# Kernel optimization log

Hardware: AMD Instinct MI355X
Metric: run time of the kernel (lower is better)

## Reference

```python
import jax, jax.numpy as jnp
import numpy as np

N, E, D = 100000, 1600000, 128


def setup_inputs() -> dict:
    key = jax.random.key(0)
    ks = jax.random.split(key, 8)
    s = 1.0 / np.sqrt(D)
    return {
        "x": jax.random.normal(ks[0], (N, D), dtype=jnp.float32),
        "edge_index": jax.random.randint(ks[1], (2, E), 0, N, dtype=jnp.int64),
        "x_prev": jax.random.normal(ks[2], (N, D), dtype=jnp.float32),
        # GCNConv params: weight [in,out], bias [out]
        "W": jax.random.uniform(ks[3], (D, D), jnp.float32, -s, s),
        "b": jnp.zeros((D,), jnp.float32),
        # GRUCell params (torch layout): [3*H, H] gates ordered (r, z, n)
        "W_ih": jax.random.uniform(ks[4], (3 * D, D), jnp.float32, -s, s),
        "W_hh": jax.random.uniform(ks[5], (3 * D, D), jnp.float32, -s, s),
        "b_ih": jax.random.uniform(ks[6], (3 * D,), jnp.float32, -s, s),
        "b_hh": jax.random.uniform(ks[7], (3 * D,), jnp.float32, -s, s),
    }


def _gcn_conv(x, edge_index, W, b):
    n = x.shape[0]
    loop = jnp.arange(n, dtype=edge_index.dtype)
    src = jnp.concatenate([edge_index[0], loop])  # [E+N]
    dst = jnp.concatenate([edge_index[1], loop])
    # symmetric normalization: deg over destinations (incl. self loops)
    deg = jax.ops.segment_sum(jnp.ones_like(dst, dtype=x.dtype), dst, num_segments=n)
    dinv = jnp.where(deg > 0, jax.lax.rsqrt(deg), 0.0)
    norm = dinv[src] * dinv[dst]  # [E+N]
    xw = x @ W  # [N, out]
    msg = xw[src] * norm[:, None]  # gather + scale
    return jax.ops.segment_sum(msg, dst, num_segments=n) + b


def _gru_cell(inp, h, W_ih, W_hh, b_ih, b_hh):
    gi = inp @ W_ih.T + b_ih  # [N, 3H]
    gh = h @ W_hh.T + b_hh
    i_r, i_z, i_n = jnp.split(gi, 3, axis=-1)
    h_r, h_z, h_n = jnp.split(gh, 3, axis=-1)
    r = jax.nn.sigmoid(i_r + h_r)
    z = jax.nn.sigmoid(i_z + h_z)
    ntil = jnp.tanh(i_n + r * h_n)
    return (1.0 - z) * ntil + z * h


def reference(x, edge_index, x_prev, W, b, W_ih, W_hh, b_ih, b_hh):
    h_cur = _gcn_conv(x, edge_index, W, b)
    return _gru_cell(h_cur, x_prev, W_ih, W_hh, b_ih, b_hh)
```

## Files before the change

kernel.cpp:

```cpp
#include <hip/hip_runtime.h>
#include <hip/hip_bf16.h>
#include <math.h>

#define DIM 128
#define PSHIFT 10
#define PSZ 1024
#define CHUNK 2048

typedef __attribute__((ext_vector_type(8))) short bf16x8;
typedef __attribute__((ext_vector_type(4))) float f32x4;
typedef unsigned short u16;
typedef unsigned int u32;
typedef unsigned long long u64;

__device__ __forceinline__ u16 f2bf(float x) {
    u32 u = __builtin_bit_cast(u32, x);
    u += 0x7fff + ((u >> 16) & 1);
    return (u16)(u >> 16);
}
__device__ __forceinline__ float bf2f(u16 h) {
    return __builtin_bit_cast(float, (u32)h << 16);
}
__device__ __forceinline__ float fsig(float x) {
    return __builtin_amdgcn_rcpf(1.f + __expf(-x));
}
__device__ __forceinline__ float ftanh(float x) {
    return 1.f - 2.f * __builtin_amdgcn_rcpf(__expf(2.f * x) + 1.f);
}


__global__ __launch_bounds__(256) void k_zero(int* __restrict__ p, int n) {
    int i = blockIdx.x * 256 + threadIdx.x;
    if (i < n) p[i] = 0;
}

__global__ __launch_bounds__(256) void k_pcount(const int* __restrict__ edst,
                                                int* __restrict__ pcnt, int E) {
    __shared__ int h[128];
    int t = threadIdx.x;
    if (t < 128) h[t] = 0;
    __syncthreads();
    int stride = gridDim.x * 256;
    for (int e = blockIdx.x * 256 + t; e < E; e += stride)
        atomicAdd(&h[edst[e] >> PSHIFT], 1);
    __syncthreads();
    if (t < 128 && h[t]) atomicAdd(&pcnt[t], h[t]);
}

__global__ __launch_bounds__(256) void k_pscan(const int* __restrict__ pcnt,
                                               int* __restrict__ poff,
                                               int* __restrict__ pfill,
                                               int* __restrict__ rowp,
                                               int P, int N, int E) {
    __shared__ int a[256];
    int t = threadIdx.x;
    int v = (t < P) ? pcnt[t] : 0;
    a[t] = v;
    __syncthreads();
    #pragma unroll
    for (int off = 1; off < 256; off <<= 1) {
        int y = (t >= off) ? a[t - off] : 0;
        __syncthreads();
        a[t] += y;
        __syncthreads();
    }
    int excl = a[t] - v;
    if (t < P) { poff[t] = excl; pfill[t] = excl; }
    if (t == 0) { poff[P] = E; rowp[N] = E; }
}

__global__ __launch_bounds__(256) void k_pscatter(const int* __restrict__ esrc,
                                                  const int* __restrict__ edst,
                                                  int* __restrict__ pfill,
                                                  u64* __restrict__ pbuf, int E) {
    __shared__ int hist[128], sc[128], lofs[128], gbase[128];
    __shared__ u32 ss[CHUNK], sd[CHUNK];
    int t = threadIdx.x;
    int c0 = blockIdx.x * CHUNK;
    int cnt = E - c0; if (cnt > CHUNK) cnt = CHUNK;

    if (t < 128) hist[t] = 0;
    __syncthreads();

    u32 s[8], d[8];
    int p[8], r[8];
    #pragma unroll
    for (int j = 0; j < 8; ++j) {
        int i = j * 256 + t;
        if (i < cnt) {
            s[j] = (u32)esrc[c0 + i];
            d[j] = (u32)edst[c0 + i];
            p[j] = (int)(d[j] >> PSHIFT);
            r[j] = atomicAdd(&hist[p[j]], 1);
        }
    }
    __syncthreads();

    if (t < 128) sc[t] = hist[t];
    __syncthreads();
    #pragma unroll
    for (int off = 1; off < 128; off <<= 1) {
        int y = 0;
        if (t < 128 && t >= off) y = sc[t - off];
        __syncthreads();
        if (t < 128) sc[t] += y;
        __syncthreads();
    }
    if (t < 128) {
        lofs[t] = sc[t] - hist[t];
        if (hist[t] > 0) gbase[t] = atomicAdd(&pfill[t], hist[t]);
    }
    __syncthreads();

    #pragma unroll
    for (int j = 0; j < 8; ++j) {
        int i = j * 256 + t;
        if (i < cnt) {
            int idx = lofs[p[j]] + r[j];
            ss[idx] = s[j];
            sd[idx] = d[j];
        }
    }
    __syncthreads();

    for (int i = t; i < cnt; i += 256) {
        u32 dd = sd[i];
        int pp = (int)(dd >> PSHIFT);
        int gpos = gbase[pp] + (i - lofs[pp]);
        pbuf[gpos] = (u64)ss[i] | ((u64)dd << 32);
    }
}

__global__ __launch_bounds__(256) void k_pfill(const u64* __restrict__ pbuf,
                                               const int* __restrict__ poff,
                                               int* __restrict__ rowp,
                                               int* __restrict__ srcs,
                                               float* __restrict__ dinv, int N) {
    __shared__ int cnt[PSZ];
    __shared__ int wsum[4];
    int p = blockIdx.x, t = threadIdx.x;
    int lane = t & 63, wid = t >> 6;
    int nb0 = p << PSHIFT;
    int ncnt = N - nb0; if (ncnt > PSZ) ncnt = PSZ;
    int b0 = poff[p], b1 = poff[p + 1];
    int bc = b1 - b0;

    for (int i = t; i < PSZ; i += 256) cnt[i] = 0;
    __syncthreads();
    for (int i = t; i < bc; i += 256) {
        u32 d = (u32)(pbuf[b0 + i] >> 32);
        atomicAdd(&cnt[d - nb0], 1);
    }
    __syncthreads();

    int base = t * 4;
    int c[4];
    int ssum = 0;
    #pragma unroll
    for (int j = 0; j < 4; ++j) { c[j] = cnt[base + j]; ssum += c[j]; }
    int incl = ssum;
    #pragma unroll
    for (int off = 1; off < 64; off <<= 1) {
        int y = __shfl_up(incl, off, 64);
        if (lane >= off) incl += y;
    }
    if (lane == 63) wsum[wid] = incl;
    __syncthreads();
    int add = 0;
    for (int w = 0; w < wid; ++w) add += wsum[w];
    int rr = b0 + add + (incl - ssum);
    #pragma unroll
    for (int j = 0; j < 4; ++j) {
        int i = base + j;
        if (i < ncnt) {
            rowp[nb0 + i] = rr;
            dinv[nb0 + i] = rsqrtf((float)(c[j] + 1));
        }
        cnt[i] = rr;
        rr += c[j];
    }
    __syncthreads();

    for (int i = t; i < bc; i += 256) {
        u64 v = pbuf[b0 + i];
        u32 sv = (u32)v;
        u32 d = (u32)(v >> 32);
        int pos = atomicAdd(&cnt[d - nb0], 1);
        srcs[pos] = (int)sv;
    }
}


__global__ __launch_bounds__(256) void k_prep(const float* __restrict__ W,
                                              const float* __restrict__ Wih,
                                              const float* __restrict__ Whh,
                                              const float4* __restrict__ xp,
                                              u16* __restrict__ Wt,
                                              u16* __restrict__ Wihb,
                                              u16* __restrict__ Whhb,
                                              u32* __restrict__ Xpb, int n4) {
    int gid = blockIdx.x * 256 + threadIdx.x;
    int stride = gridDim.x * 256;
    for (int i = gid; i < n4; i += stride) {
        float4 v = xp[i];
        Xpb[i * 2 + 0] = (u32)f2bf(v.x) | ((u32)f2bf(v.y) << 16);
        Xpb[i * 2 + 1] = (u32)f2bf(v.z) | ((u32)f2bf(v.w) << 16);
    }
    if (gid < 128 * 128) {
        int k = gid >> 7, c = gid & 127;
        Wt[c * 128 + k] = f2bf(W[gid]);
    }
    if (gid < 3 * 128 * 128) {
        Wihb[gid] = f2bf(Wih[gid]);
        Whhb[gid] = f2bf(Whh[gid]);
    }
}


__global__ __launch_bounds__(256) void k_gemm1(const float* __restrict__ X,
                                               const u16* __restrict__ Wt,
                                               u16* __restrict__ XWb, int n) {
    __shared__ u16 Wlds[128 * 128];
    int t = threadIdx.x, w = t >> 6, l = t & 63;
    int lr = l & 15, q = l >> 4;

    for (int cidx = t; cidx < 2048; cidx += 256) {
        int r = cidx >> 4, kc = cidx & 15;
        int dst = r * 128 + ((kc * 8) ^ ((r & 7) << 3));
        *(bf16x8*)(Wlds + dst) = *(const bf16x8*)(Wt + r * 128 + kc * 8);
    }
    __syncthreads();

    int r0 = blockIdx.x * 128;
    int wrow0 = r0 + w * 32;
    int sw = (lr & 7) << 3;
    int ar0 = wrow0 + lr;      if (ar0 > n - 1) ar0 = n - 1;
    int ar1 = wrow0 + 16 + lr; if (ar1 > n - 1) ar1 = n - 1;
    const float* x0 = X + (size_t)ar0 * DIM;
    const float* x1 = X + (size_t)ar1 * DIM;

    f32x4 acc[2][8];
    #pragma unroll
    for (int s = 0; s < 2; ++s)
        #pragma unroll
        for (int c = 0; c < 8; ++c) acc[s][c] = (f32x4){0.f, 0.f, 0.f, 0.f};

    #pragma unroll
    for (int kb = 0; kb < 4; ++kb) {
        int ko = kb * 32 + q * 8;
        float4 f00 = *(const float4*)(x0 + ko), f01 = *(const float4*)(x0 + ko + 4);
        float4 f10 = *(const float4*)(x1 + ko), f11 = *(const float4*)(x1 + ko + 4);
        bf16x8 a0, a1;
        a0[0] = (short)f2bf(f00.x); a0[1] = (short)f2bf(f00.y);
        a0[2] = (short)f2bf(f00.z); a0[3] = (short)f2bf(f00.w);
        a0[4] = (short)f2bf(f01.x); a0[5] = (short)f2bf(f01.y);
        a0[6] = (short)f2bf(f01.z); a0[7] = (short)f2bf(f01.w);
        a1[0] = (short)f2bf(f10.x); a1[1] = (short)f2bf(f10.y);
        a1[2] = (short)f2bf(f10.z); a1[3] = (short)f2bf(f10.w);
        a1[4] = (short)f2bf(f11.x); a1[5] = (short)f2bf(f11.y);
        a1[6] = (short)f2bf(f11.z); a1[7] = (short)f2bf(f11.w);
        int kw = ko ^ sw;
        #pragma unroll
        for (int ct = 0; ct < 8; ++ct) {
            bf16x8 b = *(const bf16x8*)(Wlds + (ct * 16 + lr) * 128 + kw);
            acc[0][ct] = __builtin_amdgcn_mfma_f32_16x16x32_bf16(a0, b, acc[0][ct], 0, 0, 0);
            acc[1][ct] = __builtin_amdgcn_mfma_f32_16x16x32_bf16(a1, b, acc[1][ct], 0, 0, 0);
        }
    }

    #pragma unroll
    for (int s = 0; s < 2; ++s)
        #pragma unroll
        for (int ct = 0; ct < 8; ++ct)
            #pragma unroll
            for (int i = 0; i < 4; ++i) {
                int row = wrow0 + s * 16 + q * 4 + i;
                if (row < n)
                    XWb[(size_t)row * DIM + ct * 16 + lr] = f2bf(acc[s][ct][i]);
            }
}


__global__ __launch_bounds__(256) void k_gather(const u16* __restrict__ XWb,
                                                const float* __restrict__ dinv,
                                                const int* __restrict__ row_ptr,
                                                const int* __restrict__ srcs,
                                                const float* __restrict__ bias,
                                                u16* __restrict__ Hcb, int n) {
    int node = blockIdx.x * 4 + (threadIdx.x >> 6);
    if (node >= n) return;
    int lane = threadIdx.x & 63;
    int c = lane * 2;

    float di = dinv[node];
    u32 sv = *(const u32*)(XWb + (size_t)node * DIM + c);
    float accx = bias[c]     + bf2f((u16)(sv & 0xffff)) * di * di;
    float accy = bias[c + 1] + bf2f((u16)(sv >> 16))    * di * di;

    int e = row_ptr[node], end = row_ptr[node + 1];
    for (; e + 7 < end; e += 8) {
        int sdx[8]; float nw[8]; u32 vv[8];
        #pragma unroll
        for (int j = 0; j < 8; ++j) sdx[j] = srcs[e + j];
        #pragma unroll
        for (int j = 0; j < 8; ++j) nw[j] = dinv[sdx[j]] * di;
        #pragma unroll
        for (int j = 0; j < 8; ++j)
            vv[j] = *(const u32*)(XWb + (size_t)sdx[j] * DIM + c);
        #pragma unroll
        for (int j = 0; j < 8; ++j) {
            accx += bf2f((u16)(vv[j] & 0xffff)) * nw[j];
            accy += bf2f((u16)(vv[j] >> 16)) * nw[j];
        }
    }
    for (; e < end; ++e) {
        int s = srcs[e];
        float nrm = dinv[s] * di;
        u32 v = *(const u32*)(XWb + (size_t)s * DIM + c);
        accx += bf2f((u16)(v & 0xffff)) * nrm;
        accy += bf2f((u16)(v >> 16)) * nrm;
    }
    *(u32*)(Hcb + (size_t)node * DIM + c) = (u32)f2bf(accx) | ((u32)f2bf(accy) << 16);
}


__global__ __launch_bounds__(256) void k_gru(const u16* __restrict__ Hcb,
                                             const u16* __restrict__ Xpb,
                                             const u16* __restrict__ Wihb,
                                             const u16* __restrict__ Whhb,
                                             const float* __restrict__ bih,
                                             const float* __restrict__ bhh,
                                             float* __restrict__ Out, int n) {
    __shared__ u16 Wlds[96 * 128];
    int t = threadIdx.x, w = t >> 6, l = t & 63;
    int lr = l & 15, q = l >> 4;

    int nwg = gridDim.x;
    int qq = nwg >> 3, rr8 = nwg & 7;
    int xcd = blockIdx.x & 7, idx = blockIdx.x >> 3;
    int logical = (xcd < rr8 ? xcd * (qq + 1) : rr8 * (qq + 1) + (xcd - rr8) * qq) + idx;
    int cs = logical & 7;
    int slot = logical >> 3;
    int nslot = nwg >> 3;
    int c0 = cs * 16;

    for (int cidx = t; cidx < 1536; cidx += 256) {
        int r = cidx >> 4, kc = cidx & 15;
        int m = (r >= 48);
        int rr = m ? r - 48 : r;
        int g = rr >> 4, cc = rr & 15;
        const u16* src = (m ? Whhb : Wihb) + (size_t)((g << 7) + c0 + cc) * DIM + kc * 8;
        int dst = r * 128 + ((kc * 8) ^ ((r & 7) << 3));
        *(bf16x8*)(Wlds + dst) = *(const bf16x8*)src;
    }
    __syncthreads();

    int sw = (lr & 7) << 3;
    int j = c0 + lr;
    float br = bih[j],       bz = bih[128 + j], bn = bih[256 + j];
    float cr = bhh[j],       cz = bhh[128 + j], cn = bhh[256 + j];

    int nrb = (n + 63) >> 6;
    for (int rb = slot; rb < nrb; rb += nslot) {
        int wrow0 = rb * 64 + w * 16;
        int ar = wrow0 + lr; if (ar > n - 1) ar = n - 1;
        const u16* hb = Hcb + (size_t)ar * DIM;
        const u16* xb = Xpb + (size_t)ar * DIM;

        u16 hp16[4];
        #pragma unroll
        for (int i = 0; i < 4; ++i) {
            int row = wrow0 + q * 4 + i; if (row > n - 1) row = n - 1;
            hp16[i] = Xpb[(size_t)row * DIM + j];
        }

        f32x4 aI[3], aH[3];
        #pragma unroll
        for (int g = 0; g < 3; ++g) {
            aI[g] = (f32x4){0.f, 0.f, 0.f, 0.f};
            aH[g] = (f32x4){0.f, 0.f, 0.f, 0.f};
        }

        #pragma unroll
        for (int kb = 0; kb < 4; ++kb) {
            int ko = kb * 32 + q * 8;
            bf16x8 hA = *(const bf16x8*)(hb + ko);
            bf16x8 xA = *(const bf16x8*)(xb + ko);
            int kw = ko ^ sw;
            #pragma unroll
            for (int g = 0; g < 3; ++g) {
                int ridx = (g * 16 + lr) * 128 + kw;
                bf16x8 bI = *(const bf16x8*)(Wlds + ridx);
                bf16x8 bH = *(const bf16x8*)(Wlds + ridx + 48 * 128);
                aI[g] = __builtin_amdgcn_mfma_f32_16x16x32_bf16(hA, bI, aI[g], 0, 0, 0);
                aH[g] = __builtin_amdgcn_mfma_f32_16x16x32_bf16(xA, bH, aH[g], 0, 0, 0);
            }
        }

        #pragma unroll
        for (int i = 0; i < 4; ++i) {
            int row = wrow0 + q * 4 + i;
            if (row >= n) continue;
            float ir = aI[0][i] + br;
            float iz = aI[1][i] + bz;
            float in_ = aI[2][i] + bn;
            float hr = aH[0][i] + cr;
            float hz = aH[1][i] + cz;
            float hn = aH[2][i] + cn;
            float rg = fsig(ir + hr);
            float zg = fsig(iz + hz);
            float ng = ftanh(in_ + rg * hn);
            float hp = bf2f(hp16[i]);
            Out[(size_t)row * DIM + j] = (1.f - zg) * ng + zg * hp;
        }
    }
}


extern "C" void kernel_launch(void* const* d_in, const int* in_sizes, int n_in,
                              void* d_out, int out_size, void* d_ws, size_t ws_size,
                              hipStream_t stream) {
    const float* x     = (const float*)d_in[0];
    const int*   ei    = (const int*)d_in[1];
    const float* xprev = (const float*)d_in[2];
    const float* W     = (const float*)d_in[3];
    const float* b     = (const float*)d_in[4];
    const float* Wih   = (const float*)d_in[5];
    const float* Whh   = (const float*)d_in[6];
    const float* bih   = (const float*)d_in[7];
    const float* bhh   = (const float*)d_in[8];

    int N = in_sizes[0] / DIM;
    int E = in_sizes[1] / 2;
    int P = (N + PSZ - 1) >> PSHIFT;
    const int* esrc = ei;
    const int* edst = ei + E;

    char* p = (char*)d_ws;
    auto alloc = [&](size_t bytes) {
        char* q = p;
        p += (bytes + 255) & ~(size_t)255;
        return q;
    };
    float* dinv = (float*)alloc((size_t)N * 4);
    int*   rowp = (int*)  alloc((size_t)(N + 1) * 4);
    int*   srcs = (int*)  alloc((size_t)E * 4);
    u16*   Hcb  = (u16*)  alloc((size_t)N * DIM * 2);
    u16*   Xpb  = (u16*)  alloc((size_t)N * DIM * 2);
    u16*   XWb  = (u16*)  alloc((size_t)N * DIM * 2);
    u16*   Wt   = (u16*)  alloc(128 * 128 * 2);
    u16*   Wihb = (u16*)  alloc(3 * 128 * 128 * 2);
    u16*   Whhb = (u16*)  alloc(3 * 128 * 128 * 2);
    int*   pcnt = (int*)  alloc(128 * 4);
    int*   poff = (int*)  alloc(129 * 4);
    int*   pfil = (int*)  alloc(128 * 4);
    u64*   pbuf = (u64*)XWb;
    float* out  = (float*)d_out;

    k_zero    <<<1, 256, 0, stream>>>(pcnt, 128);
    k_pcount  <<<1024, 256, 0, stream>>>(edst, pcnt, E);
    k_pscan   <<<1, 256, 0, stream>>>(pcnt, poff, pfil, rowp, P, N, E);
    int nch = (E + CHUNK - 1) / CHUNK;
    k_pscatter<<<nch, 256, 0, stream>>>(esrc, edst, pfil, pbuf, E);
    k_pfill   <<<P, 256, 0, stream>>>(pbuf, poff, rowp, srcs, dinv, N);
    int n4 = N * DIM / 4;
    k_prep    <<<2048, 256, 0, stream>>>(W, Wih, Whh, (const float4*)xprev,
                                         Wt, Wihb, Whhb, (u32*)Xpb, n4);
    int nrb = (N + 127) / 128;
    k_gemm1   <<<nrb, 256, 0, stream>>>(x, Wt, XWb, N);
    k_gather  <<<(N + 3) / 4, 256, 0, stream>>>(XWb, dinv, rowp, srcs, b, Hcb, N);
    k_gru     <<<1536, 256, 0, stream>>>(Hcb, Xpb, Wihb, Whhb, bih, bhh, out, N);
}
```

Before: 274.5 us.

## Gather prescaled FP8 XW rows, keep GRU weights in registers, enlarge scatter chunk

The first GEMM now multiplies each output row by dinv[src] and stores XW as FP8 instead of bf16. The gather then only sums neighbour rows and applies dinv[dst] and the bias once at the end, which halves the bytes fetched per edge and removes the per-edge dinv lookup. The GRU kernel loads its weight fragments straight into registers instead of staging them in LDS, and the scatter chunk size is doubled. FP8 storage costs noticeable precision in the aggregated features, and holding the weights in registers raises register pressure.

```diff
diff --git a/kernel.cpp b/kernel.cpp
--- a/kernel.cpp
+++ b/kernel.cpp
@@ -5,11 +5,13 @@
 #define DIM 128
 #define PSHIFT 10
 #define PSZ 1024
-#define CHUNK 2048
+#define CHUNK 4096
 
 typedef __attribute__((ext_vector_type(8))) short bf16x8;
 typedef __attribute__((ext_vector_type(4))) float f32x4;
+typedef __attribute__((ext_vector_type(2))) float f32x2;
 typedef unsigned short u16;
+typedef unsigned char u8;
 typedef unsigned int u32;
 typedef unsigned long long u64;
 
@@ -26,6 +28,10 @@
 }
 __device__ __forceinline__ float ftanh(float x) {
     return 1.f - 2.f * __builtin_amdgcn_rcpf(__expf(2.f * x) + 1.f);
+}
+__device__ __forceinline__ u8 f2fp8(float v) {
+    int pk = __builtin_amdgcn_cvt_pk_fp8_f32(v, v, 0, false);
+    return (u8)(pk & 0xff);
 }
 
 
@@ -82,10 +88,10 @@
     if (t < 128) hist[t] = 0;
     __syncthreads();
 
-    u32 s[8], d[8];
-    int p[8], r[8];
-    #pragma unroll
-    for (int j = 0; j < 8; ++j) {
+    u32 s[16], d[16];
+    int p[16], r[16];
+    #pragma unroll
+    for (int j = 0; j < 16; ++j) {
         int i = j * 256 + t;
         if (i < cnt) {
             s[j] = (u32)esrc[c0 + i];
@@ -113,7 +119,7 @@
     __syncthreads();
 
     #pragma unroll
-    for (int j = 0; j < 8; ++j) {
+    for (int j = 0; j < 16; ++j) {
         int i = j * 256 + t;
         if (i < cnt) {
             int idx = lofs[p[j]] + r[j];
@@ -219,7 +225,8 @@
 
 __global__ __launch_bounds__(256) void k_gemm1(const float* __restrict__ X,
                                                const u16* __restrict__ Wt,
-                                               u16* __restrict__ XWb, int n) {
+                                               const float* __restrict__ dinv,
+                                               u8* __restrict__ XW8, int n) {
     __shared__ u16 Wlds[128 * 128];
     int t = threadIdx.x, w = t >> 6, l = t & 63;
     int lr = l & 15, q = l >> 4;
@@ -268,6 +275,14 @@
         }
     }
 
+    float dv[2][4];
+    #pragma unroll
+    for (int s = 0; s < 2; ++s)
+        #pragma unroll
+        for (int i = 0; i < 4; ++i) {
+            int row = wrow0 + s * 16 + q * 4 + i; if (row > n - 1) row = n - 1;
+            dv[s][i] = dinv[row];
+        }
     #pragma unroll
     for (int s = 0; s < 2; ++s)
         #pragma unroll
@@ -276,12 +291,12 @@
             for (int i = 0; i < 4; ++i) {
                 int row = wrow0 + s * 16 + q * 4 + i;
                 if (row < n)
-                    XWb[(size_t)row * DIM + ct * 16 + lr] = f2bf(acc[s][ct][i]);
+                    XW8[(size_t)row * DIM + ct * 16 + lr] = f2fp8(acc[s][ct][i] * dv[s][i]);
             }
 }
 
 
-__global__ __launch_bounds__(256) void k_gather(const u16* __restrict__ XWb,
+__global__ __launch_bounds__(256) void k_gather(const u8* __restrict__ XW8,
                                                 const float* __restrict__ dinv,
                                                 const int* __restrict__ row_ptr,
                                                 const int* __restrict__ srcs,
@@ -292,35 +307,35 @@
     int lane = threadIdx.x & 63;
     int c = lane * 2;
 
-    float di = dinv[node];
-    u32 sv = *(const u32*)(XWb + (size_t)node * DIM + c);
-    float accx = bias[c]     + bf2f((u16)(sv & 0xffff)) * di * di;
-    float accy = bias[c + 1] + bf2f((u16)(sv >> 16))    * di * di;
+    u16 sv = *(const u16*)(XW8 + (size_t)node * DIM + c);
+    f32x2 sf = __builtin_amdgcn_cvt_pk_f32_fp8((int)(u32)sv, false);
+    float accx = sf[0], accy = sf[1];
 
     int e = row_ptr[node], end = row_ptr[node + 1];
     for (; e + 7 < end; e += 8) {
-        int sdx[8]; float nw[8]; u32 vv[8];
+        int sdx[8]; u16 vv[8];
         #pragma unroll
         for (int j = 0; j < 8; ++j) sdx[j] = srcs[e + j];
         #pragma unroll
-        for (int j = 0; j < 8; ++j) nw[j] = dinv[sdx[j]] * di;
-        #pragma unroll
         for (int j = 0; j < 8; ++j)
-            vv[j] = *(const u32*)(XWb + (size_t)sdx[j] * DIM + c);
+            vv[j] = *(const u16*)(XW8 + (size_t)sdx[j] * DIM + c);
         #pragma unroll
         for (int j = 0; j < 8; ++j) {
-            accx += bf2f((u16)(vv[j] & 0xffff)) * nw[j];
-            accy += bf2f((u16)(vv[j] >> 16)) * nw[j];
+            f32x2 f = __builtin_amdgcn_cvt_pk_f32_fp8((int)(u32)vv[j], false);
+            accx += f[0];
+            accy += f[1];
         }
     }
     for (; e < end; ++e) {
-        int s = srcs[e];
-        float nrm = dinv[s] * di;
-        u32 v = *(const u32*)(XWb + (size_t)s * DIM + c);
-        accx += bf2f((u16)(v & 0xffff)) * nrm;
-        accy += bf2f((u16)(v >> 16)) * nrm;
-    }
-    *(u32*)(Hcb + (size_t)node * DIM + c) = (u32)f2bf(accx) | ((u32)f2bf(accy) << 16);
+        u16 v = *(const u16*)(XW8 + (size_t)srcs[e] * DIM + c);
+        f32x2 f = __builtin_amdgcn_cvt_pk_f32_fp8((int)(u32)v, false);
+        accx += f[0];
+        accy += f[1];
+    }
+    float di = dinv[node];
+    float ox = accx * di + bias[c];
+    float oy = accy * di + bias[c + 1];
+    *(u32*)(Hcb + (size_t)node * DIM + c) = (u32)f2bf(ox) | ((u32)f2bf(oy) << 16);
 }
 
 
@@ -331,7 +346,6 @@
                                              const float* __restrict__ bih,
                                              const float* __restrict__ bhh,
                                              float* __restrict__ Out, int n) {
-    __shared__ u16 Wlds[96 * 128];
     int t = threadIdx.x, w = t >> 6, l = t & 63;
     int lr = l & 15, q = l >> 4;
 
@@ -344,18 +358,16 @@
     int nslot = nwg >> 3;
     int c0 = cs * 16;
 
-    for (int cidx = t; cidx < 1536; cidx += 256) {
-        int r = cidx >> 4, kc = cidx & 15;
-        int m = (r >= 48);
-        int rr = m ? r - 48 : r;
-        int g = rr >> 4, cc = rr & 15;
-        const u16* src = (m ? Whhb : Wihb) + (size_t)((g << 7) + c0 + cc) * DIM + kc * 8;
-        int dst = r * 128 + ((kc * 8) ^ ((r & 7) << 3));
-        *(bf16x8*)(Wlds + dst) = *(const bf16x8*)src;
-    }
-    __syncthreads();
-
-    int sw = (lr & 7) << 3;
+    bf16x8 bI[4][3], bH[4][3];
+    #pragma unroll
+    for (int kb = 0; kb < 4; ++kb)
+        #pragma unroll
+        for (int g = 0; g < 3; ++g) {
+            size_t off = (size_t)(g * 128 + c0 + lr) * DIM + kb * 32 + q * 8;
+            bI[kb][g] = *(const bf16x8*)(Wihb + off);
+            bH[kb][g] = *(const bf16x8*)(Whhb + off);
+        }
+
     int j = c0 + lr;
     float br = bih[j],       bz = bih[128 + j], bn = bih[256 + j];
     float cr = bhh[j],       cz = bhh[128 + j], cn = bhh[256 + j];
@@ -386,14 +398,10 @@
             int ko = kb * 32 + q * 8;
             bf16x8 hA = *(const bf16x8*)(hb + ko);
             bf16x8 xA = *(const bf16x8*)(xb + ko);
-            int kw = ko ^ sw;
             #pragma unroll
             for (int g = 0; g < 3; ++g) {
-                int ridx = (g * 16 + lr) * 128 + kw;
-                bf16x8 bI = *(const bf16x8*)(Wlds + ridx);
-                bf16x8 bH = *(const bf16x8*)(Wlds + ridx + 48 * 128);
-                aI[g] = __builtin_amdgcn_mfma_f32_16x16x32_bf16(hA, bI, aI[g], 0, 0, 0);
-                aH[g] = __builtin_amdgcn_mfma_f32_16x16x32_bf16(xA, bH, aH[g], 0, 0, 0);
+                aI[g] = __builtin_amdgcn_mfma_f32_16x16x32_bf16(hA, bI[kb][g], aI[g], 0, 0, 0);
+                aH[g] = __builtin_amdgcn_mfma_f32_16x16x32_bf16(xA, bH[kb][g], aH[g], 0, 0, 0);
             }
         }
 
@@ -447,14 +455,16 @@
     int*   srcs = (int*)  alloc((size_t)E * 4);
     u16*   Hcb  = (u16*)  alloc((size_t)N * DIM * 2);
     u16*   Xpb  = (u16*)  alloc((size_t)N * DIM * 2);
-    u16*   XWb  = (u16*)  alloc((size_t)N * DIM * 2);
+    size_t xwsz = (size_t)N * DIM;
+    size_t pbsz = (size_t)E * 8;
+    u8*    XW8  = (u8*)   alloc(xwsz > pbsz ? xwsz : pbsz);
     u16*   Wt   = (u16*)  alloc(128 * 128 * 2);
     u16*   Wihb = (u16*)  alloc(3 * 128 * 128 * 2);
     u16*   Whhb = (u16*)  alloc(3 * 128 * 128 * 2);
     int*   pcnt = (int*)  alloc(128 * 4);
     int*   poff = (int*)  alloc(129 * 4);
     int*   pfil = (int*)  alloc(128 * 4);
-    u64*   pbuf = (u64*)XWb;
+    u64*   pbuf = (u64*)XW8;
     float* out  = (float*)d_out;
 
     k_zero    <<<1, 256, 0, stream>>>(pcnt, 128);
@@ -467,7 +477,7 @@
     k_prep    <<<2048, 256, 0, stream>>>(W, Wih, Whh, (const float4*)xprev,
                                          Wt, Wihb, Whhb, (u32*)Xpb, n4);
     int nrb = (N + 127) / 128;
-    k_gemm1   <<<nrb, 256, 0, stream>>>(x, Wt, XWb, N);
-    k_gather  <<<(N + 3) / 4, 256, 0, stream>>>(XWb, dinv, rowp, srcs, b, Hcb, N);
+    k_gemm1   <<<nrb, 256, 0, stream>>>(x, Wt, dinv, XW8, N);
+    k_gather  <<<(N + 3) / 4, 256, 0, stream>>>(XW8, dinv, rowp, srcs, b, Hcb, N);
     k_gru     <<<1536, 256, 0, stream>>>(Hcb, Xpb, Wihb, Whhb, bih, bhh, out, N);
 }
```

Result: no change. 273.2 us (-0.5%).
